# Performance work log

Hardware: AMD Instinct MI355X
Metric: run time of the kernel (lower is better)

## Reference

```python
import jax, jax.numpy as jnp
import numpy as np

B, S, D, H = 2, 2048, 1024, 16
HD = D // H


def setup_inputs() -> dict:
    key = jax.random.key(0)
    ks = jax.random.split(key, 9)
    std = 0.02
    return {
        "x": jax.random.normal(ks[0], (B, S, D), dtype=jnp.float32),
        "wq": jax.random.normal(ks[1], (D, D), dtype=jnp.float32) * std,
        "bq": jnp.zeros((D,), dtype=jnp.float32),
        "wk": jax.random.normal(ks[2], (D, D), dtype=jnp.float32) * std,
        "bk": jnp.zeros((D,), dtype=jnp.float32),
        "wv": jax.random.normal(ks[3], (D, D), dtype=jnp.float32) * std,
        "bv": jnp.zeros((D,), dtype=jnp.float32),
        "wo": jax.random.normal(ks[4], (D, D), dtype=jnp.float32) * std,
        "bo": jnp.zeros((D,), dtype=jnp.float32),
    }


def reference(x, wq, bq, wk, bk, wv, bv, wo, bo):
    bsz, seq_len, d_model = x.shape
    # projections: torch Linear computes x @ W.T + b with W of shape (out, in)
    q = (x @ wq.T + bq).reshape(bsz, seq_len, H, HD).transpose(0, 2, 1, 3)  # bhsd
    k = (x @ wk.T + bk).reshape(bsz, seq_len, H, HD).transpose(0, 2, 1, 3)
    v = (x @ wv.T + bv).reshape(bsz, seq_len, H, HD).transpose(0, 2, 1, 3)
    scale = HD ** -0.5
    scores = jnp.einsum("bhqd,bhkd->bhqk", q, k) * scale  # [B,H,S,S]
    causal = jnp.tril(jnp.ones((seq_len, seq_len), dtype=bool))
    scores = jnp.where(causal[None, None], scores, -jnp.inf)
    attn = jax.nn.softmax(scores, axis=-1)
    ctx = jnp.einsum("bhqk,bhkd->bhqd", attn, v)
    ctx = ctx.transpose(0, 2, 1, 3).reshape(bsz, seq_len, d_model)
    return ctx @ wo.T + bo
```

## Files before the change

kernel.cpp:

```cpp
#include <hip/hip_runtime.h>
#include <hip/hip_bf16.h>

#define B_  2
#define S_  2048
#define D_  1024
#define H_  16
#define HD_ 64
#define M_  (B_ * S_)

typedef __bf16 bf16;
typedef __bf16 bf16x4 __attribute__((ext_vector_type(4)));
typedef __bf16 bf16x8 __attribute__((ext_vector_type(8)));
typedef float  f32x4  __attribute__((ext_vector_type(4)));

__device__ __forceinline__ bf16x8 ld8g(const bf16* p) { return *(const bf16x8*)p; }

#define GLL(g, l) __builtin_amdgcn_global_load_lds( \
    (const __attribute__((address_space(1))) void*)(g), \
    (__attribute__((address_space(3))) void*)(l), 16, 0, 0)

__global__ __launch_bounds__(256) void convert_kernel(
    const float* __restrict__ x,  const float* __restrict__ wq,
    const float* __restrict__ wk, const float* __restrict__ wv,
    const float* __restrict__ wo,
    bf16* __restrict__ xb,  bf16* __restrict__ wqb, bf16* __restrict__ wkb,
    bf16* __restrict__ wvb, bf16* __restrict__ wob)
{
    const int seg = blockIdx.y;
    const float* src;
    bf16* dst;
    if (seg < 4)      { src = x  + (long)seg * 1048576; dst = xb  + (long)seg * 1048576; }
    else if (seg == 4){ src = wq; dst = wqb; }
    else if (seg == 5){ src = wk; dst = wkb; }
    else if (seg == 6){ src = wv; dst = wvb; }
    else              { src = wo; dst = wob; }
    const long i = ((long)blockIdx.x * 256 + threadIdx.x) * 8;
    float4 a = *(const float4*)(src + i);
    float4 b = *(const float4*)(src + i + 4);
    bf16x8 r;
    r[0] = (bf16)a.x; r[1] = (bf16)a.y; r[2] = (bf16)a.z; r[3] = (bf16)a.w;
    r[4] = (bf16)b.x; r[5] = (bf16)b.y; r[6] = (bf16)b.z; r[7] = (bf16)b.w;
    *(bf16x8*)(dst + i) = r;
}

__device__ __forceinline__ void gemm_acc_bk32(
    const bf16* __restrict__ A, const bf16* __restrict__ Bt,
    f32x4 (&acc)[4][4])
{
    __shared__ bf16 As[128 * 32];
    __shared__ bf16 Bs[128 * 32];

    const int tid  = threadIdx.x;
    const int wave = tid >> 6;
    const int lane = tid & 63;
    const int quad = lane >> 4;
    const int l15  = lane & 15;
    const int wr   = (wave >> 1) * 64;
    const int wc   = (wave & 1) * 64;
    const int m0   = blockIdx.y * 128;
    const int n0   = blockIdx.x * 128;

    const int sr = wave * 16 + (lane >> 2);
    const int sc = (lane & 3) * 8;
    const bf16* Ag = A  + (long)(m0 + sr) * D_ + sc;
    const bf16* Bg = Bt + (long)(n0 + sr) * D_ + sc;
    bf16* lA = As + wave * 512;
    bf16* lB = Bs + wave * 512;

    for (int k0 = 0; k0 < D_; k0 += 32) {
        __syncthreads();
        GLL(Ag + k0,             lA);
        GLL(Ag + 64 * D_ + k0,   lA + 64 * 32);
        GLL(Bg + k0,             lB);
        GLL(Bg + 64 * D_ + k0,   lB + 64 * 32);
        __syncthreads();

        bf16x8 af[4], bfr[4];
        for (int mi = 0; mi < 4; mi++)
            af[mi] = *(const bf16x8*)&As[(wr + mi * 16 + l15) * 32 + quad * 8];
        for (int ni = 0; ni < 4; ni++)
            bfr[ni] = *(const bf16x8*)&Bs[(wc + ni * 16 + l15) * 32 + quad * 8];

        for (int mi = 0; mi < 4; mi++)
            for (int ni = 0; ni < 4; ni++)
                acc[mi][ni] = __builtin_amdgcn_mfma_f32_16x16x32_bf16(
                    af[mi], bfr[ni], acc[mi][ni], 0, 0, 0);
    }
}

__global__ __launch_bounds__(256) void gemm_qkv(
    const bf16* __restrict__ xb,
    const bf16* __restrict__ wqb, const bf16* __restrict__ wkb, const bf16* __restrict__ wvb,
    const float* __restrict__ bq, const float* __restrict__ bk, const float* __restrict__ bv,
    bf16* __restrict__ qb, bf16* __restrict__ kb, bf16* __restrict__ vt)
{
    const bf16*  Bt   = (blockIdx.z == 0) ? wqb : (blockIdx.z == 1) ? wkb : wvb;
    const float* bias = (blockIdx.z == 0) ? bq  : (blockIdx.z == 1) ? bk  : bv;

    f32x4 acc[4][4] = {};
    gemm_acc_bk32(xb, Bt, acc);

    const int lane = threadIdx.x & 63;
    const int wave = threadIdx.x >> 6;
    const int quad = lane >> 4;
    const int l15  = lane & 15;
    const int wr   = (wave >> 1) * 64;
    const int wc   = (wave & 1) * 64;
    const int m0   = blockIdx.y * 128;
    const int n0   = blockIdx.x * 128;

    if (blockIdx.z < 2) {
        bf16* Cout = (blockIdx.z == 0) ? qb : kb;
        for (int ni = 0; ni < 4; ni++) {
            const int col = n0 + wc + ni * 16 + l15;
            const float bv = bias[col];
            for (int mi = 0; mi < 4; mi++) {
                const int rowb = m0 + wr + mi * 16 + quad * 4;
                for (int r = 0; r < 4; r++)
                    Cout[(long)(rowb + r) * D_ + col] = (bf16)(acc[mi][ni][r] + bv);
            }
        }
    } else {
        for (int ni = 0; ni < 4; ni++) {
            const int col = n0 + wc + ni * 16 + l15;
            const float bv = bias[col];
            const int h = col >> 6, hd = col & (HD_ - 1);
            for (int mi = 0; mi < 4; mi++) {
                const int rowb = m0 + wr + mi * 16 + quad * 4;
                const int b = rowb >> 11;
                const int s0 = rowb & (S_ - 1);
                bf16x4 v4;
                for (int r = 0; r < 4; r++) v4[r] = (bf16)(acc[mi][ni][r] + bv);
                *(bf16x4*)&vt[(((long)(b * H_ + h)) * HD_ + hd) * S_ + s0] = v4;
            }
        }
    }
}

__global__ __launch_bounds__(256) void gemm_out(
    const bf16* __restrict__ cb, const bf16* __restrict__ wob,
    const float* __restrict__ bo, float* __restrict__ out)
{
    f32x4 acc[4][4] = {};
    gemm_acc_bk32(cb, wob, acc);

    const int lane = threadIdx.x & 63;
    const int wave = threadIdx.x >> 6;
    const int quad = lane >> 4;
    const int l15  = lane & 15;
    const int wr   = (wave >> 1) * 64;
    const int wc   = (wave & 1) * 64;
    const int m0   = blockIdx.y * 128;
    const int n0   = blockIdx.x * 128;

    for (int ni = 0; ni < 4; ni++) {
        const int col = n0 + wc + ni * 16 + l15;
        const float bv = bo[col];
        for (int mi = 0; mi < 4; mi++) {
            const int rowb = m0 + wr + mi * 16 + quad * 4;
            for (int r = 0; r < 4; r++)
                out[(long)(rowb + r) * D_ + col] = acc[mi][ni][r] + bv;
        }
    }
}

__global__ __launch_bounds__(512) void attn_kernel(
    const bf16* __restrict__ Q, const bf16* __restrict__ K,
    const bf16* __restrict__ vt, bf16* __restrict__ ctx)
{
    constexpr int LDK = 72;
    __shared__ bf16 Ks[64 * LDK];
    __shared__ bf16 Vt[64 * LDK];
    __shared__ bf16 Pq[8][16 * LDK];

    const int tid  = threadIdx.x;
    const int wave = tid >> 6;
    const int lane = tid & 63;
    const int quad = lane >> 4;
    const int l15  = lane & 15;
    const int bh   = blockIdx.y;
    const int qt   = (blockIdx.y < 16) ? blockIdx.x : (15 - (int)blockIdx.x);
    const int b    = bh >> 4, h = bh & 15;
    const long base  = ((long)b * S_) * D_ + h * HD_;
    const bf16* Vth  = vt + (long)bh * HD_ * S_;

    const int krow = tid >> 3;
    const int kcol = (tid & 7) * 8;

    const int qw    = qt * 128 + wave * 16;
    const int qrow  = qw + l15;
    const bf16* Qr = Q + base + (long)qrow * D_;
    bf16x8 qf0 = ld8g(&Qr[quad * 8]);
    bf16x8 qf1 = ld8g(&Qr[quad * 8 + 32]);

    float l_i = 0.f;
    f32x4 o_acc[4] = {};

    auto process_tile = [&](int kbase) {
        if (kbase > qw + 15) return;
        f32x4 sc[4];
        for (int kt = 0; kt < 4; kt++) {
            const bf16* Kr = &Ks[(kt * 16 + l15) * LDK + quad * 8];
            bf16x8 a0 = *(const bf16x8*)Kr;
            bf16x8 a1 = *(const bf16x8*)(Kr + 32);
            f32x4 z = {};
            z = __builtin_amdgcn_mfma_f32_16x16x32_bf16(a0, qf0, z, 0, 0, 0);
            z = __builtin_amdgcn_mfma_f32_16x16x32_bf16(a1, qf1, z, 0, 0, 0);
            sc[kt] = z;
        }
        float sum = 0.f;
        if (kbase + 63 > qw) {
            for (int kt = 0; kt < 4; kt++)
                for (int r = 0; r < 4; r++) {
                    const int k_g = kbase + kt * 16 + quad * 4 + r;
                    const float p = (k_g <= qrow) ? __expf(sc[kt][r] * 0.125f) : 0.f;
                    sc[kt][r] = p;
                    sum += p;
                }
        } else {
            for (int kt = 0; kt < 4; kt++)
                for (int r = 0; r < 4; r++) {
                    const float p = __expf(sc[kt][r] * 0.125f);
                    sc[kt][r] = p;
                    sum += p;
                }
        }
        sum += __shfl_xor(sum, 16, 64);
        sum += __shfl_xor(sum, 32, 64);
        l_i += sum;

        bf16* Pw = &Pq[wave][0];
        for (int kt = 0; kt < 4; kt++) {
            union { uint2 u; bf16 hh[4]; } pk;
            pk.hh[0] = (bf16)sc[kt][0];
            pk.hh[1] = (bf16)sc[kt][1];
            pk.hh[2] = (bf16)sc[kt][2];
            pk.hh[3] = (bf16)sc[kt][3];
            *(uint2*)&Pw[l15 * LDK + kt * 16 + quad * 4] = pk.u;
        }
        __asm__ volatile("s_waitcnt lgkmcnt(0)" ::: "memory");
        bf16x8 pf0 = *(const bf16x8*)&Pw[l15 * LDK + quad * 8];
        bf16x8 pf1 = *(const bf16x8*)&Pw[l15 * LDK + quad * 8 + 32];

        for (int ni = 0; ni < 4; ni++) {
            const bf16* Vr = &Vt[(ni * 16 + l15) * LDK + quad * 8];
            bf16x8 av0 = *(const bf16x8*)Vr;
            bf16x8 av1 = *(const bf16x8*)(Vr + 32);
            o_acc[ni] = __builtin_amdgcn_mfma_f32_16x16x32_bf16(av0, pf0, o_acc[ni], 0, 0, 0);
            o_acc[ni] = __builtin_amdgcn_mfma_f32_16x16x32_bf16(av1, pf1, o_acc[ni], 0, 0, 0);
        }
    };

    bf16x8 kA = ld8g(K + base + (long)krow * D_ + kcol);
    bf16x8 wA = ld8g(Vth + (long)krow * S_ + kcol);
    bf16x8 kB = ld8g(K + base + (long)(64 + krow) * D_ + kcol);
    bf16x8 wB = ld8g(Vth + (long)krow * S_ + 64 + kcol);

    const int njt = 2 * qt + 2;
    for (int j = 0; j < njt; j += 2) {
        __syncthreads();
        *(bf16x8*)&Ks[krow * LDK + kcol] = kA;
        *(bf16x8*)&Vt[krow * LDK + kcol] = wA;
        if (j + 2 < njt) {
            kA = ld8g(K + base + (long)((j + 2) * 64 + krow) * D_ + kcol);
            wA = ld8g(Vth + (long)krow * S_ + (j + 2) * 64 + kcol);
        }
        __syncthreads();
        process_tile(j * 64);
        __syncthreads();
        *(bf16x8*)&Ks[krow * LDK + kcol] = kB;
        *(bf16x8*)&Vt[krow * LDK + kcol] = wB;
        if (j + 3 < njt) {
            kB = ld8g(K + base + (long)((j + 3) * 64 + krow) * D_ + kcol);
            wB = ld8g(Vth + (long)krow * S_ + (j + 3) * 64 + kcol);
        }
        __syncthreads();
        process_tile(j * 64 + 64);
    }

    const float invl = 1.f / l_i;
    bf16* Pw = &Pq[wave][0];
    for (int ni = 0; ni < 4; ni++)
        for (int r = 0; r < 4; r++)
            Pw[l15 * LDK + ni * 16 + quad * 4 + r] = (bf16)(o_acc[ni][r] * invl);
    __asm__ volatile("s_waitcnt lgkmcnt(0)" ::: "memory");
    for (int round = 0; round < 2; round++) {
        const int rowq = (lane >> 3) + round * 8;
        bf16x8 val = *(const bf16x8*)&Pw[rowq * LDK + (lane & 7) * 8];
        const int q_g = qt * 128 + wave * 16 + rowq;
        *(bf16x8*)&ctx[base + (long)q_g * D_ + (lane & 7) * 8] = val;
    }
}

extern "C" void kernel_launch(void* const* d_in, const int* in_sizes, int n_in,
                              void* d_out, int out_size, void* d_ws, size_t ws_size,
                              hipStream_t stream)
{
    const float* x  = (const float*)d_in[0];
    const float* wq = (const float*)d_in[1];
    const float* bq = (const float*)d_in[2];
    const float* wk = (const float*)d_in[3];
    const float* bk = (const float*)d_in[4];
    const float* wv = (const float*)d_in[5];
    const float* bv = (const float*)d_in[6];
    const float* wo = (const float*)d_in[7];
    const float* bo = (const float*)d_in[8];
    float* out = (float*)d_out;

    const long NX = (long)M_ * D_;
    const long NW = (long)D_ * D_;
    bf16* xb  = (bf16*)d_ws;
    bf16* wqb = xb  + NX;
    bf16* wkb = wqb + NW;
    bf16* wvb = wkb + NW;
    bf16* wob = wvb + NW;
    bf16* qb  = wob + NW;
    bf16* kb  = qb  + NX;
    bf16* vt  = kb  + NX;
    bf16* cb  = xb;

    dim3 blk(256, 1, 1);

    convert_kernel<<<dim3(512, 8), blk, 0, stream>>>(
        x, wq, wk, wv, wo, xb, wqb, wkb, wvb, wob);

    gemm_qkv<<<dim3(8, 32, 3), blk, 0, stream>>>(
        xb, wqb, wkb, wvb, bq, bk, bv, qb, kb, vt);

    attn_kernel<<<dim3(16, 32), dim3(512, 1, 1), 0, stream>>>(qb, kb, vt, cb);

    gemm_out<<<dim3(8, 32), blk, 0, stream>>>(cb, wob, bo, out);
}
```

Measured before the change: 184.6 us.

## Give each attention wave two 16-row query groups to reuse K/V fragments

The attention block drops from 8 waves to 4, and each wave now handles 32 query rows as two 16-row groups. Each K and V fragment read from shared memory feeds two MFMAs, which halves LDS traffic per unit of compute, and each thread stages twice as many K/V rows. The costs are more registers per thread (two accumulator sets, two score sets), fewer waves per block to hide latency, and coarser causal skipping, since a wave now skips a tile only when it lies beyond all 32 of its rows.

```diff
diff --git a/kernel.cpp b/kernel.cpp
--- a/kernel.cpp
+++ b/kernel.cpp
@@ -164,14 +164,14 @@
     }
 }
 
-__global__ __launch_bounds__(512) void attn_kernel(
+__global__ __launch_bounds__(256) void attn_kernel(
     const bf16* __restrict__ Q, const bf16* __restrict__ K,
     const bf16* __restrict__ vt, bf16* __restrict__ ctx)
 {
     constexpr int LDK = 72;
     __shared__ bf16 Ks[64 * LDK];
     __shared__ bf16 Vt[64 * LDK];
-    __shared__ bf16 Pq[8][16 * LDK];
+    __shared__ bf16 Pq[4][32 * LDK];
 
     const int tid  = threadIdx.x;
     const int wave = tid >> 6;
@@ -187,107 +187,142 @@
     const int krow = tid >> 3;
     const int kcol = (tid & 7) * 8;
 
-    const int qw    = qt * 128 + wave * 16;
-    const int qrow  = qw + l15;
-    const bf16* Qr = Q + base + (long)qrow * D_;
-    bf16x8 qf0 = ld8g(&Qr[quad * 8]);
-    bf16x8 qf1 = ld8g(&Qr[quad * 8 + 32]);
-
-    float l_i = 0.f;
-    f32x4 o_acc[4] = {};
+    const int qw = qt * 128 + wave * 32;
+    bf16x8 qf[2][2];
+    for (int g = 0; g < 2; g++) {
+        const bf16* Qr = Q + base + (long)(qw + g * 16 + l15) * D_;
+        qf[g][0] = ld8g(&Qr[quad * 8]);
+        qf[g][1] = ld8g(&Qr[quad * 8 + 32]);
+    }
+
+    float l_i[2] = {0.f, 0.f};
+    f32x4 o_acc[4][2] = {};
 
     auto process_tile = [&](int kbase) {
-        if (kbase > qw + 15) return;
-        f32x4 sc[4];
+        if (kbase > qw + 31) return;
+        f32x4 sc[4][2];
         for (int kt = 0; kt < 4; kt++) {
             const bf16* Kr = &Ks[(kt * 16 + l15) * LDK + quad * 8];
             bf16x8 a0 = *(const bf16x8*)Kr;
             bf16x8 a1 = *(const bf16x8*)(Kr + 32);
-            f32x4 z = {};
-            z = __builtin_amdgcn_mfma_f32_16x16x32_bf16(a0, qf0, z, 0, 0, 0);
-            z = __builtin_amdgcn_mfma_f32_16x16x32_bf16(a1, qf1, z, 0, 0, 0);
-            sc[kt] = z;
-        }
-        float sum = 0.f;
+            for (int g = 0; g < 2; g++) {
+                f32x4 z = {};
+                z = __builtin_amdgcn_mfma_f32_16x16x32_bf16(a0, qf[g][0], z, 0, 0, 0);
+                z = __builtin_amdgcn_mfma_f32_16x16x32_bf16(a1, qf[g][1], z, 0, 0, 0);
+                sc[kt][g] = z;
+            }
+        }
+        float sum[2] = {0.f, 0.f};
         if (kbase + 63 > qw) {
-            for (int kt = 0; kt < 4; kt++)
-                for (int r = 0; r < 4; r++) {
-                    const int k_g = kbase + kt * 16 + quad * 4 + r;
-                    const float p = (k_g <= qrow) ? __expf(sc[kt][r] * 0.125f) : 0.f;
-                    sc[kt][r] = p;
-                    sum += p;
-                }
+            for (int g = 0; g < 2; g++) {
+                const int qrow = qw + g * 16 + l15;
+                for (int kt = 0; kt < 4; kt++)
+                    for (int r = 0; r < 4; r++) {
+                        const int k_g = kbase + kt * 16 + quad * 4 + r;
+                        const float p = (k_g <= qrow)
+                            ? __expf(sc[kt][g][r] * 0.125f) : 0.f;
+                        sc[kt][g][r] = p;
+                        sum[g] += p;
+                    }
+            }
         } else {
-            for (int kt = 0; kt < 4; kt++)
-                for (int r = 0; r < 4; r++) {
-                    const float p = __expf(sc[kt][r] * 0.125f);
-                    sc[kt][r] = p;
-                    sum += p;
-                }
-        }
-        sum += __shfl_xor(sum, 16, 64);
-        sum += __shfl_xor(sum, 32, 64);
-        l_i += sum;
+            for (int g = 0; g < 2; g++)
+                for (int kt = 0; kt < 4; kt++)
+                    for (int r = 0; r < 4; r++) {
+                        const float p = __expf(sc[kt][g][r] * 0.125f);
+                        sc[kt][g][r] = p;
+                        sum[g] += p;
+                    }
+        }
+        for (int g = 0; g < 2; g++) {
+            float s = sum[g];
+            s += __shfl_xor(s, 16, 64);
+            s += __shfl_xor(s, 32, 64);
+            l_i[g] += s;
+        }
 
         bf16* Pw = &Pq[wave][0];
-        for (int kt = 0; kt < 4; kt++) {
-            union { uint2 u; bf16 hh[4]; } pk;
-            pk.hh[0] = (bf16)sc[kt][0];
-            pk.hh[1] = (bf16)sc[kt][1];
-            pk.hh[2] = (bf16)sc[kt][2];
-            pk.hh[3] = (bf16)sc[kt][3];
-            *(uint2*)&Pw[l15 * LDK + kt * 16 + quad * 4] = pk.u;
-        }
+        for (int g = 0; g < 2; g++)
+            for (int kt = 0; kt < 4; kt++) {
+                union { uint2 u; bf16 hh[4]; } pk;
+                pk.hh[0] = (bf16)sc[kt][g][0];
+                pk.hh[1] = (bf16)sc[kt][g][1];
+                pk.hh[2] = (bf16)sc[kt][g][2];
+                pk.hh[3] = (bf16)sc[kt][g][3];
+                *(uint2*)&Pw[(g * 16 + l15) * LDK + kt * 16 + quad * 4] = pk.u;
+            }
         __asm__ volatile("s_waitcnt lgkmcnt(0)" ::: "memory");
-        bf16x8 pf0 = *(const bf16x8*)&Pw[l15 * LDK + quad * 8];
-        bf16x8 pf1 = *(const bf16x8*)&Pw[l15 * LDK + quad * 8 + 32];
+        bf16x8 pf[2][2];
+        for (int g = 0; g < 2; g++) {
+            pf[g][0] = *(const bf16x8*)&Pq[wave][(g * 16 + l15) * LDK + quad * 8];
+            pf[g][1] = *(const bf16x8*)&Pq[wave][(g * 16 + l15) * LDK + quad * 8 + 32];
+        }
 
         for (int ni = 0; ni < 4; ni++) {
             const bf16* Vr = &Vt[(ni * 16 + l15) * LDK + quad * 8];
             bf16x8 av0 = *(const bf16x8*)Vr;
             bf16x8 av1 = *(const bf16x8*)(Vr + 32);
-            o_acc[ni] = __builtin_amdgcn_mfma_f32_16x16x32_bf16(av0, pf0, o_acc[ni], 0, 0, 0);
-            o_acc[ni] = __builtin_amdgcn_mfma_f32_16x16x32_bf16(av1, pf1, o_acc[ni], 0, 0, 0);
+            for (int g = 0; g < 2; g++) {
+                o_acc[ni][g] = __builtin_amdgcn_mfma_f32_16x16x32_bf16(av0, pf[g][0], o_acc[ni][g], 0, 0, 0);
+                o_acc[ni][g] = __builtin_amdgcn_mfma_f32_16x16x32_bf16(av1, pf[g][1], o_acc[ni][g], 0, 0, 0);
+            }
         }
     };
 
-    bf16x8 kA = ld8g(K + base + (long)krow * D_ + kcol);
-    bf16x8 wA = ld8g(Vth + (long)krow * S_ + kcol);
-    bf16x8 kB = ld8g(K + base + (long)(64 + krow) * D_ + kcol);
-    bf16x8 wB = ld8g(Vth + (long)krow * S_ + 64 + kcol);
+    bf16x8 kA0 = ld8g(K + base + (long)krow * D_ + kcol);
+    bf16x8 kA1 = ld8g(K + base + (long)(krow + 32) * D_ + kcol);
+    bf16x8 wA0 = ld8g(Vth + (long)krow * S_ + kcol);
+    bf16x8 wA1 = ld8g(Vth + (long)(krow + 32) * S_ + kcol);
+    bf16x8 kB0 = ld8g(K + base + (long)(64 + krow) * D_ + kcol);
+    bf16x8 kB1 = ld8g(K + base + (long)(64 + krow + 32) * D_ + kcol);
+    bf16x8 wB0 = ld8g(Vth + (long)krow * S_ + 64 + kcol);
+    bf16x8 wB1 = ld8g(Vth + (long)(krow + 32) * S_ + 64 + kcol);
 
     const int njt = 2 * qt + 2;
     for (int j = 0; j < njt; j += 2) {
         __syncthreads();
-        *(bf16x8*)&Ks[krow * LDK + kcol] = kA;
-        *(bf16x8*)&Vt[krow * LDK + kcol] = wA;
+        *(bf16x8*)&Ks[krow * LDK + kcol]        = kA0;
+        *(bf16x8*)&Ks[(krow + 32) * LDK + kcol] = kA1;
+        *(bf16x8*)&Vt[krow * LDK + kcol]        = wA0;
+        *(bf16x8*)&Vt[(krow + 32) * LDK + kcol] = wA1;
         if (j + 2 < njt) {
-            kA = ld8g(K + base + (long)((j + 2) * 64 + krow) * D_ + kcol);
-            wA = ld8g(Vth + (long)krow * S_ + (j + 2) * 64 + kcol);
+            const int kb2 = (j + 2) * 64;
+            kA0 = ld8g(K + base + (long)(kb2 + krow) * D_ + kcol);
+            kA1 = ld8g(K + base + (long)(kb2 + krow + 32) * D_ + kcol);
+            wA0 = ld8g(Vth + (long)krow * S_ + kb2 + kcol);
+            wA1 = ld8g(Vth + (long)(krow + 32) * S_ + kb2 + kcol);
         }
         __syncthreads();
         process_tile(j * 64);
         __syncthreads();
-        *(bf16x8*)&Ks[krow * LDK + kcol] = kB;
-        *(bf16x8*)&Vt[krow * LDK + kcol] = wB;
+        *(bf16x8*)&Ks[krow * LDK + kcol]        = kB0;
+        *(bf16x8*)&Ks[(krow + 32) * LDK + kcol] = kB1;
+        *(bf16x8*)&Vt[krow * LDK + kcol]        = wB0;
+        *(bf16x8*)&Vt[(krow + 32) * LDK + kcol] = wB1;
         if (j + 3 < njt) {
-            kB = ld8g(K + base + (long)((j + 3) * 64 + krow) * D_ + kcol);
-            wB = ld8g(Vth + (long)krow * S_ + (j + 3) * 64 + kcol);
+            const int kb3 = (j + 3) * 64;
+            kB0 = ld8g(K + base + (long)(kb3 + krow) * D_ + kcol);
+            kB1 = ld8g(K + base + (long)(kb3 + krow + 32) * D_ + kcol);
+            wB0 = ld8g(Vth + (long)krow * S_ + kb3 + kcol);
+            wB1 = ld8g(Vth + (long)(krow + 32) * S_ + kb3 + kcol);
         }
         __syncthreads();
         process_tile(j * 64 + 64);
     }
 
-    const float invl = 1.f / l_i;
     bf16* Pw = &Pq[wave][0];
-    for (int ni = 0; ni < 4; ni++)
-        for (int r = 0; r < 4; r++)
-            Pw[l15 * LDK + ni * 16 + quad * 4 + r] = (bf16)(o_acc[ni][r] * invl);
+    for (int g = 0; g < 2; g++) {
+        const float invl = 1.f / l_i[g];
+        for (int ni = 0; ni < 4; ni++)
+            for (int r = 0; r < 4; r++)
+                Pw[(g * 16 + l15) * LDK + ni * 16 + quad * 4 + r] =
+                    (bf16)(o_acc[ni][g][r] * invl);
+    }
     __asm__ volatile("s_waitcnt lgkmcnt(0)" ::: "memory");
-    for (int round = 0; round < 2; round++) {
+    for (int round = 0; round < 4; round++) {
         const int rowq = (lane >> 3) + round * 8;
         bf16x8 val = *(const bf16x8*)&Pw[rowq * LDK + (lane & 7) * 8];
-        const int q_g = qt * 128 + wave * 16 + rowq;
+        const int q_g = qw + rowq;
         *(bf16x8*)&ctx[base + (long)q_g * D_ + (lane & 7) * 8] = val;
     }
 }
@@ -327,7 +362,7 @@
     gemm_qkv<<<dim3(8, 32, 3), blk, 0, stream>>>(
         xb, wqb, wkb, wvb, bq, bk, bv, qb, kb, vt);
 
-    attn_kernel<<<dim3(16, 32), dim3(512, 1, 1), 0, stream>>>(qb, kb, vt, cb);
+    attn_kernel<<<dim3(16, 32), blk, 0, stream>>>(qb, kb, vt, cb);
 
     gemm_out<<<dim3(8, 32), blk, 0, stream>>>(cb, wob, bo, out);
 }
```

Result: no change. 187.6 us (+1.6%).
